# Performance work log

Measured on AMD Instinct MI355X. Metric: run time of the kernel, lower is better.

The kernel has to match this reference:

```python
import jax, jax.numpy as jnp
import numpy as np

B, N, C, H = 2, 8192, 256, 8  # Dh == C (attention_head_size = embedding_channels)
EPS = 1e-5  # InstanceNorm2d default eps


def setup_inputs() -> dict:
    key = jax.random.key(0)
    k1, k2, k3, k4, k5 = jax.random.split(key, 5)
    s = 1.0 / np.sqrt(C)
    return {
        "emb": jax.random.normal(k1, (B, N, C), dtype=jnp.float32),
        "Wq": jax.random.normal(k2, (C, C * H), dtype=jnp.float32) * s,
        "Wk": jax.random.normal(k3, (C, C * H), dtype=jnp.float32) * s,
        "Wv": jax.random.normal(k4, (C, C * H), dtype=jnp.float32) * s,
        "Wo": jax.random.normal(k5, (C * H, C), dtype=jnp.float32) * s,
    }


def reference(emb, Wq, Wk, Wv, Wo):
    b, n, c = emb.shape
    h = Wq.shape[1] // c  # num_heads; head_dim Dh == c

    def heads(x):  # [B,N,H*Dh] -> [B,H,N,Dh]
        return x.reshape(b, n, h, c).transpose(0, 2, 1, 3)

    qh = heads(emb @ Wq)  # [B,H,N,Dh]
    kh = heads(emb @ Wk)
    vh = heads(emb @ Wv)

    # channel attention: contract over sequence dim N -> [B,H,Dh,Dh]
    attn = jnp.einsum("bhnd,bhne->bhde", qh, kh)

    # InstanceNorm2d over the Dh x Dh map per (b,h), affine=False, biased var
    mu = attn.mean(axis=(2, 3), keepdims=True)
    var = attn.var(axis=(2, 3), keepdims=True)
    attn = (attn - mu) * jax.lax.rsqrt(var + EPS)

    attn = jax.nn.softmax(attn, axis=3)

    # attn @ v^T -> [B,H,Dh,N]
    ctx = jnp.einsum("bhde,bhne->bhdn", attn, vh)

    # permute(0,3,2,1) -> [B,N,Dh,H], flatten (Dh,H) -> KV_size
    ctx = ctx.transpose(0, 3, 2, 1).reshape(b, n, c * h)
    return ctx @ Wo  # [B,N,C]
```

## Files before the change

### kernel.cpp

```cpp
#include <hip/hip_runtime.h>
#include <hip/hip_bf16.h>

#define NB 2
#define NN 8192
#define NC 256
#define NH 8
#define NCH 2048

static constexpr float EPS = 1e-5f;


typedef __attribute__((ext_vector_type(8))) short bf16x8;
typedef __attribute__((ext_vector_type(4))) float f32x4;

#define MFMA16(a, b, c) __builtin_amdgcn_mfma_f32_16x16x32_bf16(a, b, c, 0, 0, 0)

static constexpr int ETH  = 0;
static constexpr int ETL  = 4194304;
static constexpr int WQTH = 8388608;
static constexpr int WQTL = 8912896;
static constexpr int WKTH = 9437184;
static constexpr int WKTL = 9961472;
static constexpr int WVH  = 10485760;
static constexpr int WVL  = 11010048;
static constexpr int WORH = 11534336;
static constexpr int WORL = 12058624;
static constexpr int GHH  = 12582912;
static constexpr int GHL  = 12713984;
static constexpr int T1H  = 12845056;
static constexpr int T1L  = 13893632;
static constexpr int SMH  = 14942208;
static constexpr int SML  = 15990784;
static constexpr int PTH  = 17039360;
static constexpr int PTL  = 17170432;


__device__ __forceinline__ ushort bf16rn(float x) {
    uint u = __float_as_uint(x);
    return (ushort)((u + 0x7fffu + ((u >> 16) & 1u)) >> 16);
}
__device__ __forceinline__ float bf2f(ushort h) { return __uint_as_float(((uint)h) << 16); }

__device__ __forceinline__ void stage64(ushort* __restrict__ lds, const ushort* __restrict__ src,
                                        int row0, int k0, int ld) {
    int t = threadIdx.x;
    int g = t & 7, r = t >> 3;
#pragma unroll
    for (int i = 0; i < 2; ++i, r += 32) {
        uint4 v = *(const uint4*)(src + (row0 + r) * ld + k0 + g * 8);
        *(uint4*)((char*)lds + r * 128 + ((g ^ (r & 7)) << 4)) = v;
    }
}

__device__ __forceinline__ void stage64_f32(ushort* __restrict__ ldsh, ushort* __restrict__ ldsl,
                                            const float* __restrict__ src, int row0, int k0, int ld) {
    int t = threadIdx.x;
    int g = t & 15, r = t >> 4;
#pragma unroll
    for (int i = 0; i < 4; ++i, r += 16) {
        float4 v = *(const float4*)(src + (row0 + r) * ld + k0 + g * 4);
        ushort h0 = bf16rn(v.x), h1 = bf16rn(v.y), h2 = bf16rn(v.z), h3 = bf16rn(v.w);
        ushort e0 = bf16rn(v.x - bf2f(h0)), e1 = bf16rn(v.y - bf2f(h1));
        ushort e2 = bf16rn(v.z - bf2f(h2)), e3 = bf16rn(v.w - bf2f(h3));
        int byte = r * 128 + ((((g >> 1) ^ (r & 7)) << 4) | ((g & 1) << 3));
        ushort4 hv = {h0, h1, h2, h3}, lv = {e0, e1, e2, e3};
        *(ushort4*)((char*)ldsh + byte) = hv;
        *(ushort4*)((char*)ldsl + byte) = lv;
    }
}

__device__ __forceinline__ bf16x8 frag64(const ushort* __restrict__ lds, int rbase, int ks) {
    int l = threadIdx.x & 63;
    int r = rbase + (l & 15);
    int slot = (ks * 4 + (l >> 4)) ^ (r & 7);
    return *(const bf16x8*)((const char*)lds + r * 128 + slot * 16);
}

__device__ __forceinline__ void mac3(f32x4& acc, bf16x8 ah, bf16x8 al, bf16x8 bh, bf16x8 bl) {
    acc = MFMA16(ah, bh, acc);
    acc = MFMA16(ah, bl, acc);
    acc = MFMA16(al, bh, acc);
}

__device__ __forceinline__ void mfma_tile(const ushort* Ah, const ushort* Al,
                                          const ushort* Bh, const ushort* Bl,
                                          int wm, int wn, f32x4 acc[2][2]) {
#pragma unroll
    for (int ks = 0; ks < 2; ++ks) {
        bf16x8 ah[2], al[2], bh[2], bl[2];
        ah[0] = frag64(Ah, wm, ks);      ah[1] = frag64(Ah, wm + 16, ks);
        al[0] = frag64(Al, wm, ks);      al[1] = frag64(Al, wm + 16, ks);
        bh[0] = frag64(Bh, wn, ks);      bh[1] = frag64(Bh, wn + 16, ks);
        bl[0] = frag64(Bl, wn, ks);      bl[1] = frag64(Bl, wn + 16, ks);
#pragma unroll
        for (int mi = 0; mi < 2; ++mi)
#pragma unroll
            for (int ni = 0; ni < 2; ++ni)
                mac3(acc[mi][ni], ah[mi], al[mi], bh[ni], bl[ni]);
    }
}

__device__ __forceinline__ void gemm_core(const ushort* Ahi, const ushort* Alo, int arow0, int lda, int k0a,
                                          const ushort* Bhi, const ushort* Blo, int brow0, int ldb, int k0b,
                                          int nkt, ushort* lds, f32x4 acc[2][2]) {
    ushort* Ah = lds; ushort* Al = lds + 4096; ushort* Bh = lds + 8192; ushort* Bl = lds + 12288;
    int w = threadIdx.x >> 6;
    int wm = (w >> 1) * 32, wn = (w & 1) * 32;
    for (int t = 0; t < nkt; ++t) {
        stage64(Ah, Ahi, arow0, k0a + t * 64, lda);
        stage64(Al, Alo, arow0, k0a + t * 64, lda);
        stage64(Bh, Bhi, brow0, k0b + t * 64, ldb);
        stage64(Bl, Blo, brow0, k0b + t * 64, ldb);
        __syncthreads();
        mfma_tile(Ah, Al, Bh, Bl, wm, wn, acc);
        __syncthreads();
    }
}

__device__ __forceinline__ void ep_hilo(ushort* Dh, ushort* Dl, int ld, int row0, int col0, f32x4 acc[2][2]) {
    int l = threadIdx.x & 63, w = threadIdx.x >> 6;
    int wm = (w >> 1) * 32, wn = (w & 1) * 32;
#pragma unroll
    for (int mi = 0; mi < 2; ++mi)
#pragma unroll
        for (int ni = 0; ni < 2; ++ni)
#pragma unroll
            for (int r = 0; r < 4; ++r) {
                float x = acc[mi][ni][r];
                int idx = (row0 + wm + mi * 16 + (l >> 4) * 4 + r) * ld + col0 + wn + ni * 16 + (l & 15);
                ushort h = bf16rn(x);
                Dh[idx] = h;
                Dl[idx] = bf16rn(x - bf2f(h));
            }
}

__device__ __forceinline__ void ep_f32(float* D, int ld, int row0, int col0, f32x4 acc[2][2]) {
    int l = threadIdx.x & 63, w = threadIdx.x >> 6;
    int wm = (w >> 1) * 32, wn = (w & 1) * 32;
#pragma unroll
    for (int mi = 0; mi < 2; ++mi)
#pragma unroll
        for (int ni = 0; ni < 2; ++ni)
#pragma unroll
            for (int r = 0; r < 4; ++r)
                D[(row0 + wm + mi * 16 + (l >> 4) * 4 + r) * ld + col0 + wn + ni * 16 + (l & 15)] = acc[mi][ni][r];
}

__device__ __forceinline__ void tsplit(uint (*lds)[65], const float* __restrict__ src, int srcStride,
                                       ushort* __restrict__ DH, ushort* __restrict__ DL) {
    int t = threadIdx.x;
    int r = t >> 4, g = t & 15;
#pragma unroll
    for (int i = 0; i < 4; ++i) {
        int m = r + i * 16;
        float4 v = *(const float4*)(src + m * srcStride + g * 4);
        ushort h;
        h = bf16rn(v.x); lds[g * 4 + 0][m] = h | ((uint)bf16rn(v.x - bf2f(h)) << 16);
        h = bf16rn(v.y); lds[g * 4 + 1][m] = h | ((uint)bf16rn(v.y - bf2f(h)) << 16);
        h = bf16rn(v.z); lds[g * 4 + 2][m] = h | ((uint)bf16rn(v.z - bf2f(h)) << 16);
        h = bf16rn(v.w); lds[g * 4 + 3][m] = h | ((uint)bf16rn(v.w - bf2f(h)) << 16);
    }
    __syncthreads();
    int j = t >> 3, q = t & 7;
#pragma unroll
    for (int i = 0; i < 2; ++i) {
        int jj = j + i * 32;
        uint a0 = lds[jj][q * 8 + 0], a1 = lds[jj][q * 8 + 1], a2 = lds[jj][q * 8 + 2], a3 = lds[jj][q * 8 + 3];
        uint a4 = lds[jj][q * 8 + 4], a5 = lds[jj][q * 8 + 5], a6 = lds[jj][q * 8 + 6], a7 = lds[jj][q * 8 + 7];
        uint4 hv = {(a0 & 0xffffu) | (a1 << 16), (a2 & 0xffffu) | (a3 << 16),
                    (a4 & 0xffffu) | (a5 << 16), (a6 & 0xffffu) | (a7 << 16)};
        uint4 lv = {(a0 >> 16) | (a1 & 0xffff0000u), (a2 >> 16) | (a3 & 0xffff0000u),
                    (a4 >> 16) | (a5 & 0xffff0000u), (a6 >> 16) | (a7 & 0xffff0000u)};
        *(uint4*)(DH + jj * NC + q * 8) = hv;
        *(uint4*)(DL + jj * NC + q * 8) = lv;
    }
}


__global__ __launch_bounds__(256) void k_prep(const float* __restrict__ wq, const float* __restrict__ wk,
                                              const float* __restrict__ wv, const float* __restrict__ wo,
                                              ushort* __restrict__ us, float* __restrict__ stats) {
    __shared__ uint lds[64][65];
    int x = blockIdx.x, z = blockIdx.y;
    int t = threadIdx.x;
    if (z == 3) {
        if (x == 0 && t < 64) stats[t] = 0.f;
        int i = (x * 256 + t) * 4;
        float4 v = *(const float4*)(wv + i);
        ushort h0 = bf16rn(v.x), h1 = bf16rn(v.y), h2 = bf16rn(v.z), h3 = bf16rn(v.w);
        ushort e0 = bf16rn(v.x - bf2f(h0)), e1 = bf16rn(v.y - bf2f(h1));
        ushort e2 = bf16rn(v.z - bf2f(h2)), e3 = bf16rn(v.w - bf2f(h3));
        ushort4 hv = {h0, h1, h2, h3}, lv = {e0, e1, e2, e3};
        *(ushort4*)(us + WVH + i) = hv;
        *(ushort4*)(us + WVL + i) = lv;
        return;
    }
    if (x >= 128) return;
    if (z == 2) {
        int h = x >> 4, dt = (x >> 2) & 3, jt = x & 3;
        tsplit(lds, wo + (dt * 64 * 8 + h) * NC + jt * 64, 8 * NC,
               us + WORH + h * 65536 + (jt * 64) * NC + dt * 64,
               us + WORL + h * 65536 + (jt * 64) * NC + dt * 64);
        return;
    }
    int jt = x >> 2, ct = x & 3;
    const float* W = z ? wk : wq;
    int dh = (z ? WKTH : WQTH) + (jt * 64) * NC + ct * 64;
    int dl = (z ? WKTL : WQTL) + (jt * 64) * NC + ct * 64;
    tsplit(lds, W + (ct * 64) * NCH + jt * 64, NCH, us + dh, us + dl);
}

__global__ __launch_bounds__(256) void k_s0(const float* __restrict__ emb, ushort* __restrict__ us) {
    __shared__ uint lds[64][65];
    int nt = blockIdx.x, ct = blockIdx.y, b = blockIdx.z;
    int t = threadIdx.x;
    const float* E = emb + b * (NN * NC);
    int n0 = nt * 64, c0 = ct * 64;
    int r = t >> 4, g = t & 15;
#pragma unroll
    for (int i = 0; i < 4; ++i) {
        int n = r + i * 16;
        float4 v = *(const float4*)(E + (n0 + n) * NC + c0 + g * 4);
        ushort h;
        h = bf16rn(v.x); lds[g * 4 + 0][n] = h | ((uint)bf16rn(v.x - bf2f(h)) << 16);
        h = bf16rn(v.y); lds[g * 4 + 1][n] = h | ((uint)bf16rn(v.y - bf2f(h)) << 16);
        h = bf16rn(v.z); lds[g * 4 + 2][n] = h | ((uint)bf16rn(v.z - bf2f(h)) << 16);
        h = bf16rn(v.w); lds[g * 4 + 3][n] = h | ((uint)bf16rn(v.w - bf2f(h)) << 16);
    }
    __syncthreads();
    ushort* EH = us + ETH + b * (NC * NN);
    ushort* EL = us + ETL + b * (NC * NN);
    int c = t >> 3, q = t & 7;
#pragma unroll
    for (int i = 0; i < 2; ++i) {
        int cc = c + i * 32;
        uint a0 = lds[cc][q * 8 + 0], a1 = lds[cc][q * 8 + 1], a2 = lds[cc][q * 8 + 2], a3 = lds[cc][q * 8 + 3];
        uint a4 = lds[cc][q * 8 + 4], a5 = lds[cc][q * 8 + 5], a6 = lds[cc][q * 8 + 6], a7 = lds[cc][q * 8 + 7];
        uint4 hv = {(a0 & 0xffffu) | (a1 << 16), (a2 & 0xffffu) | (a3 << 16),
                    (a4 & 0xffffu) | (a5 << 16), (a6 & 0xffffu) | (a7 << 16)};
        uint4 lv = {(a0 >> 16) | (a1 & 0xffff0000u), (a2 >> 16) | (a3 & 0xffff0000u),
                    (a4 >> 16) | (a5 & 0xffff0000u), (a6 >> 16) | (a7 & 0xffff0000u)};
        *(uint4*)(EH + (c0 + cc) * NN + n0 + q * 8) = hv;
        *(uint4*)(EL + (c0 + cc) * NN + n0 + q * 8) = lv;
    }
}

static __device__ const int TI1[10] = {0, 0, 0, 0, 1, 1, 1, 2, 2, 3};
static __device__ const int TI2[10] = {0, 1, 2, 3, 1, 2, 3, 2, 3, 3};

__global__ __launch_bounds__(256) void k_gram(const ushort* __restrict__ us, float* __restrict__ gp) {
    __shared__ ushort lds[16384];
    ushort* Ah = lds; ushort* Al = lds + 4096; ushort* Bh = lds + 8192; ushort* Bl = lds + 12288;
    int tile = blockIdx.x, kc = blockIdx.y, b = blockIdx.z;
    int c1 = TI1[tile] * 64, c2 = TI2[tile] * 64;
    bool diag = (c1 == c2);
    const ushort* eh = us + ETH + b * (NC * NN);
    const ushort* el = us + ETL + b * (NC * NN);
    int w = threadIdx.x >> 6;
    int wm = (w >> 1) * 32, wn = (w & 1) * 32;
    f32x4 acc[2][2] = {{{0.f, 0.f, 0.f, 0.f}, {0.f, 0.f, 0.f, 0.f}},
                       {{0.f, 0.f, 0.f, 0.f}, {0.f, 0.f, 0.f, 0.f}}};
    for (int kb = 0; kb < 8; ++kb) {
        int n0 = kc * 512 + kb * 64;
        stage64(Ah, eh, c1, n0, NN);
        stage64(Al, el, c1, n0, NN);
        if (!diag) { stage64(Bh, eh, c2, n0, NN); stage64(Bl, el, c2, n0, NN); }
        __syncthreads();
        mfma_tile(Ah, Al, diag ? Ah : Bh, diag ? Al : Bl, wm, wn, acc);
        __syncthreads();
    }
    ep_f32(gp + ((b * 16 + kc) * 10 + tile) * 4096, 64, 0, 0, acc);
}

__global__ __launch_bounds__(256) void k_s2(const float* __restrict__ gp, ushort* __restrict__ us) {
    __shared__ float T[64][65];
    int tile = blockIdx.x, b = blockIdx.y;
    int c1 = TI1[tile] * 64, c2 = TI2[tile] * 64;
    int t = threadIdx.x;
    const float* src = gp + (b * 160 + tile) * 4096;
    ushort* GH = us + GHH + b * 65536;
    ushort* GL = us + GHL + b * 65536;
    float4 s[4] = {{0.f, 0.f, 0.f, 0.f}, {0.f, 0.f, 0.f, 0.f}, {0.f, 0.f, 0.f, 0.f}, {0.f, 0.f, 0.f, 0.f}};
    for (int kc = 0; kc < 16; ++kc) {
        const float4* p = (const float4*)(src + kc * 40960);
#pragma unroll
        for (int k2 = 0; k2 < 4; ++k2) {
            float4 v = p[t + k2 * 256];
            s[k2].x += v.x; s[k2].y += v.y; s[k2].z += v.z; s[k2].w += v.w;
        }
    }
#pragma unroll
    for (int k2 = 0; k2 < 4; ++k2) {
        int f = t + k2 * 256;
        int r = f >> 4, c = (f & 15) * 4;
        ushort h0 = bf16rn(s[k2].x), h1 = bf16rn(s[k2].y), h2 = bf16rn(s[k2].z), h3 = bf16rn(s[k2].w);
        ushort e0 = bf16rn(s[k2].x - bf2f(h0)), e1 = bf16rn(s[k2].y - bf2f(h1));
        ushort e2 = bf16rn(s[k2].z - bf2f(h2)), e3 = bf16rn(s[k2].w - bf2f(h3));
        ushort4 hv = {h0, h1, h2, h3}, lv = {e0, e1, e2, e3};
        *(ushort4*)(GH + (c1 + r) * NC + c2 + c) = hv;
        *(ushort4*)(GL + (c1 + r) * NC + c2 + c) = lv;
        T[r][c + 0] = s[k2].x; T[r][c + 1] = s[k2].y; T[r][c + 2] = s[k2].z; T[r][c + 3] = s[k2].w;
    }
    if (c1 != c2) {
        __syncthreads();
#pragma unroll
        for (int k2 = 0; k2 < 4; ++k2) {
            int f = t + k2 * 256;
            int r = f >> 4, c = (f & 15) * 4;
            float a0 = T[c + 0][r], a1 = T[c + 1][r], a2 = T[c + 2][r], a3 = T[c + 3][r];
            ushort h0 = bf16rn(a0), h1 = bf16rn(a1), h2 = bf16rn(a2), h3 = bf16rn(a3);
            ushort e0 = bf16rn(a0 - bf2f(h0)), e1 = bf16rn(a1 - bf2f(h1));
            ushort e2 = bf16rn(a2 - bf2f(h2)), e3 = bf16rn(a3 - bf2f(h3));
            ushort4 hv = {h0, h1, h2, h3}, lv = {e0, e1, e2, e3};
            *(ushort4*)(GH + (c2 + r) * NC + c1 + c) = hv;
            *(ushort4*)(GL + (c2 + r) * NC + c1 + c) = lv;
        }
    }
}

__global__ __launch_bounds__(256) void k_t1(ushort* __restrict__ us) {
    __shared__ ushort lds[16384];
    int mt = blockIdx.x, nt = blockIdx.y, b = blockIdx.z;
    f32x4 acc[2][2] = {{{0.f, 0.f, 0.f, 0.f}, {0.f, 0.f, 0.f, 0.f}},
                       {{0.f, 0.f, 0.f, 0.f}, {0.f, 0.f, 0.f, 0.f}}};
    gemm_core(us + WQTH, us + WQTL, mt * 64, NC, 0,
              us + GHH + b * 65536, us + GHL + b * 65536, nt * 64, NC, 0, 4, lds, acc);
    ep_hilo(us + T1H + b * 524288, us + T1L + b * 524288, NC, mt * 64, nt * 64, acc);
}

__global__ __launch_bounds__(256) void k_attn(ushort* __restrict__ us, float* __restrict__ attn,
                                              float* __restrict__ stats) {
    __shared__ ushort lds[16384];
    int tile = blockIdx.x, bh = blockIdx.y;
    int b = bh >> 3, h = bh & 7;
    int row0 = (tile >> 2) * 64, col0 = (tile & 3) * 64;
    f32x4 acc[2][2] = {{{0.f, 0.f, 0.f, 0.f}, {0.f, 0.f, 0.f, 0.f}},
                       {{0.f, 0.f, 0.f, 0.f}, {0.f, 0.f, 0.f, 0.f}}};
    gemm_core(us + T1H + b * 524288, us + T1L + b * 524288, h * 256 + row0, NC, 0,
              us + WKTH, us + WKTL, h * 256 + col0, NC, 0, 4, lds, acc);
    float* D = attn + bh * 65536;
    int l = threadIdx.x & 63, w = threadIdx.x >> 6;
    int wm = (w >> 1) * 32, wn = (w & 1) * 32;
    float lsum = 0.f, lss = 0.f;
#pragma unroll
    for (int mi = 0; mi < 2; ++mi)
#pragma unroll
        for (int ni = 0; ni < 2; ++ni)
#pragma unroll
            for (int r = 0; r < 4; ++r) {
                float x = acc[mi][ni][r];
                D[(row0 + wm + mi * 16 + (l >> 4) * 4 + r) * NC + col0 + wn + ni * 16 + (l & 15)] = x;
                lsum += x; lss += x * x;
            }
#pragma unroll
    for (int o = 32; o > 0; o >>= 1) { lsum += __shfl_xor(lsum, o); lss += __shfl_xor(lss, o); }
    if (l == 0) { atomicAdd(&stats[bh * 2], lsum); atomicAdd(&stats[bh * 2 + 1], lss); }
}

__global__ __launch_bounds__(256) void k_sm(const float* __restrict__ attn, const float* __restrict__ stats,
                                            ushort* __restrict__ us) {
    int bh = blockIdx.x, rb = blockIdx.y;
    float mean = stats[bh * 2] * (1.f / 65536.f);
    float var = stats[bh * 2 + 1] * (1.f / 65536.f) - mean * mean;
    float rs = rsqrtf(var + EPS);
    int w = threadIdx.x >> 6, l = threadIdx.x & 63;
    const float* src = attn + bh * 65536;
    ushort* dh = us + SMH + bh * 65536;
    ushort* dl = us + SML + bh * 65536;
    for (int rr = 0; rr < 16; ++rr) {
        int row = rb * 64 + w * 16 + rr;
        float4 v = *(const float4*)(src + row * 256 + l * 4);
        v.x *= rs; v.y *= rs; v.z *= rs; v.w *= rs;
        float mx = fmaxf(fmaxf(v.x, v.y), fmaxf(v.z, v.w));
#pragma unroll
        for (int o = 32; o > 0; o >>= 1) mx = fmaxf(mx, __shfl_xor(mx, o));
        float e0 = __expf(v.x - mx), e1 = __expf(v.y - mx), e2 = __expf(v.z - mx), e3 = __expf(v.w - mx);
        float se = e0 + e1 + e2 + e3;
#pragma unroll
        for (int o = 32; o > 0; o >>= 1) se += __shfl_xor(se, o);
        float inv = 1.f / se;
        e0 *= inv; e1 *= inv; e2 *= inv; e3 *= inv;
        ushort h0 = bf16rn(e0), h1 = bf16rn(e1), h2 = bf16rn(e2), h3 = bf16rn(e3);
        ushort f0 = bf16rn(e0 - bf2f(h0)), f1 = bf16rn(e1 - bf2f(h1));
        ushort f2 = bf16rn(e2 - bf2f(h2)), f3 = bf16rn(e3 - bf2f(h3));
        ushort4 hv = {h0, h1, h2, h3}, lv = {f0, f1, f2, f3};
        *(ushort4*)(dh + row * 256 + l * 4) = hv;
        *(ushort4*)(dl + row * 256 + l * 4) = lv;
    }
}

__global__ __launch_bounds__(256) void k_m(ushort* __restrict__ us) {
    __shared__ ushort lds[16384];
    int tile = blockIdx.x, bh = blockIdx.y;
    int h = bh & 7;
    int c0 = (tile >> 2) * 64, d0 = (tile & 3) * 64;
    f32x4 acc[2][2] = {{{0.f, 0.f, 0.f, 0.f}, {0.f, 0.f, 0.f, 0.f}},
                       {{0.f, 0.f, 0.f, 0.f}, {0.f, 0.f, 0.f, 0.f}}};
    gemm_core(us + WVH, us + WVL, c0, NCH, h * 256,
              us + SMH + bh * 65536, us + SML + bh * 65536, d0, NC, 0, 4, lds, acc);
    ep_hilo(us + T1H + bh * 65536, us + T1L + bh * 65536, NC, c0, d0, acc);
}

__global__ __launch_bounds__(256) void k_pt(ushort* __restrict__ us, float* __restrict__ ptp) {
    __shared__ ushort lds[16384];
    int tile = blockIdx.x, bh = blockIdx.y;
    int h = bh & 7;
    int j0 = (tile >> 2) * 64, c0 = (tile & 3) * 64;
    f32x4 acc[2][2] = {{{0.f, 0.f, 0.f, 0.f}, {0.f, 0.f, 0.f, 0.f}},
                       {{0.f, 0.f, 0.f, 0.f}, {0.f, 0.f, 0.f, 0.f}}};
    gemm_core(us + WORH + h * 65536, us + WORL + h * 65536, j0, NC, 0,
              us + T1H + bh * 65536, us + T1L + bh * 65536, c0, NC, 0, 4, lds, acc);
    ep_f32(ptp + bh * 65536, NC, j0, c0, acc);
}

__global__ __launch_bounds__(256) void k_s4(const float* __restrict__ ptp, ushort* __restrict__ us) {
    int b = blockIdx.y;
    int i = (blockIdx.x * 256 + threadIdx.x) * 4;
    const float* src = ptp + b * 8 * 65536 + i;
    float4 s = {0.f, 0.f, 0.f, 0.f};
#pragma unroll
    for (int h = 0; h < 8; ++h) {
        float4 v = *(const float4*)(src + h * 65536);
        s.x += v.x; s.y += v.y; s.z += v.z; s.w += v.w;
    }
    ushort h0 = bf16rn(s.x), h1 = bf16rn(s.y), h2 = bf16rn(s.z), h3 = bf16rn(s.w);
    ushort e0 = bf16rn(s.x - bf2f(h0)), e1 = bf16rn(s.y - bf2f(h1));
    ushort e2 = bf16rn(s.z - bf2f(h2)), e3 = bf16rn(s.w - bf2f(h3));
    ushort4 hv = {h0, h1, h2, h3}, lv = {e0, e1, e2, e3};
    *(ushort4*)(us + PTH + b * 65536 + i) = hv;
    *(ushort4*)(us + PTL + b * 65536 + i) = lv;
}

__global__ __launch_bounds__(256) void k_out(const float* __restrict__ emb, const ushort* __restrict__ us,
                                             float* __restrict__ out) {
    __shared__ ushort lds[16384];
    ushort* Ah = lds; ushort* Al = lds + 4096; ushort* Bh = lds + 8192; ushort* Bl = lds + 12288;
    int nt = blockIdx.x, jt = blockIdx.y, b = blockIdx.z;
    const float* E = emb + b * (NN * NC);
    const ushort* PH = us + PTH + b * 65536;
    const ushort* PL = us + PTL + b * 65536;
    int w = threadIdx.x >> 6;
    int wm = (w >> 1) * 32, wn = (w & 1) * 32;
    f32x4 acc[2][2] = {{{0.f, 0.f, 0.f, 0.f}, {0.f, 0.f, 0.f, 0.f}},
                       {{0.f, 0.f, 0.f, 0.f}, {0.f, 0.f, 0.f, 0.f}}};
    for (int t = 0; t < 4; ++t) {
        stage64_f32(Ah, Al, E, nt * 64, t * 64, NC);
        stage64(Bh, PH, jt * 64, t * 64, NC);
        stage64(Bl, PL, jt * 64, t * 64, NC);
        __syncthreads();
        mfma_tile(Ah, Al, Bh, Bl, wm, wn, acc);
        __syncthreads();
    }
    ep_f32(out + b * (NN * NC), NC, nt * 64, jt * 64, acc);
}


extern "C" void kernel_launch(void* const* d_in, const int* in_sizes, int n_in,
                              void* d_out, int out_size, void* d_ws, size_t ws_size,
                              hipStream_t stream) {
    const float* emb = (const float*)d_in[0];
    const float* Wq  = (const float*)d_in[1];
    const float* Wk  = (const float*)d_in[2];
    const float* Wv  = (const float*)d_in[3];
    const float* Wo  = (const float*)d_in[4];
    float* out = (float*)d_out;
    float* ws  = (float*)d_ws;

    float* Gp    = ws;
    float* attn  = ws;
    float* Ptp   = ws + 1310720;
    float* stats = ws + 2359296;
    ushort* us   = (ushort*)(ws + 2359360);

    k_prep<<<dim3(512, 4),     dim3(256), 0, stream>>>(Wq, Wk, Wv, Wo, us, stats);
    k_s0  <<<dim3(128, 4, NB), dim3(256), 0, stream>>>(emb, us);
    k_gram<<<dim3(10, 16, NB), dim3(256), 0, stream>>>(us, Gp);
    k_s2  <<<dim3(10, NB),     dim3(256), 0, stream>>>(Gp, us);
    k_t1  <<<dim3(32, 4, NB),  dim3(256), 0, stream>>>(us);
    k_attn<<<dim3(16, 16),     dim3(256), 0, stream>>>(us, attn, stats);
    k_sm  <<<dim3(16, 4),      dim3(256), 0, stream>>>(attn, stats, us);
    k_m   <<<dim3(16, 16),     dim3(256), 0, stream>>>(us);
    k_pt  <<<dim3(16, 16),     dim3(256), 0, stream>>>(us, Ptp);
    k_s4  <<<dim3(64, NB),     dim3(256), 0, stream>>>(Ptp, us);
    k_out <<<dim3(128, 4, NB), dim3(256), 0, stream>>>(emb, us, out);
}
```

Before: 172.6 us.

## Merge emb split into prep, atomically reduce P, and widen gram/softmax grids

Folds the emb transpose/hi-lo split kernel into k_prep as extra grid planes, and has k_prep zero a P buffer. k_pt now accumulates per-head contributions into P with float atomics, which removes the k_s4 reduction kernel; k_out then splits P from fp32 itself. The Gram kernel gets twice as many K-chunks with half the depth each to raise parallelism, and the softmax kernel handles 4 rows per wave over a larger grid. Together these cut launches and intermediate traffic, at the cost of atomic contention, nondeterministic summation order, and a larger partial-sum reduction in k_s2.

```diff
diff --git a/kernel.cpp b/kernel.cpp
--- a/kernel.cpp
+++ b/kernel.cpp
@@ -31,8 +31,6 @@
 static constexpr int T1L  = 13893632;
 static constexpr int SMH  = 14942208;
 static constexpr int SML  = 15990784;
-static constexpr int PTH  = 17039360;
-static constexpr int PTL  = 17170432;
 
 
 __device__ __forceinline__ ushort bf16rn(float x) {
@@ -179,12 +177,47 @@
 
 __global__ __launch_bounds__(256) void k_prep(const float* __restrict__ wq, const float* __restrict__ wk,
                                               const float* __restrict__ wv, const float* __restrict__ wo,
-                                              ushort* __restrict__ us, float* __restrict__ stats) {
+                                              const float* __restrict__ emb, ushort* __restrict__ us,
+                                              float* __restrict__ P, float* __restrict__ stats) {
     __shared__ uint lds[64][65];
     int x = blockIdx.x, z = blockIdx.y;
     int t = threadIdx.x;
+    if (z >= 4) {
+        int b = z - 4, nt = x >> 2, ct = x & 3;
+        const float* E = emb + b * (NN * NC);
+        int n0 = nt * 64, c0 = ct * 64;
+        int r = t >> 4, g = t & 15;
+#pragma unroll
+        for (int i = 0; i < 4; ++i) {
+            int n = r + i * 16;
+            float4 v = *(const float4*)(E + (n0 + n) * NC + c0 + g * 4);
+            ushort h;
+            h = bf16rn(v.x); lds[g * 4 + 0][n] = h | ((uint)bf16rn(v.x - bf2f(h)) << 16);
+            h = bf16rn(v.y); lds[g * 4 + 1][n] = h | ((uint)bf16rn(v.y - bf2f(h)) << 16);
+            h = bf16rn(v.z); lds[g * 4 + 2][n] = h | ((uint)bf16rn(v.z - bf2f(h)) << 16);
+            h = bf16rn(v.w); lds[g * 4 + 3][n] = h | ((uint)bf16rn(v.w - bf2f(h)) << 16);
+        }
+        __syncthreads();
+        ushort* EH = us + ETH + b * (NC * NN);
+        ushort* EL = us + ETL + b * (NC * NN);
+        int c = t >> 3, q = t & 7;
+#pragma unroll
+        for (int i = 0; i < 2; ++i) {
+            int cc = c + i * 32;
+            uint a0 = lds[cc][q * 8 + 0], a1 = lds[cc][q * 8 + 1], a2 = lds[cc][q * 8 + 2], a3 = lds[cc][q * 8 + 3];
+            uint a4 = lds[cc][q * 8 + 4], a5 = lds[cc][q * 8 + 5], a6 = lds[cc][q * 8 + 6], a7 = lds[cc][q * 8 + 7];
+            uint4 hv = {(a0 & 0xffffu) | (a1 << 16), (a2 & 0xffffu) | (a3 << 16),
+                        (a4 & 0xffffu) | (a5 << 16), (a6 & 0xffffu) | (a7 << 16)};
+            uint4 lv = {(a0 >> 16) | (a1 & 0xffff0000u), (a2 >> 16) | (a3 & 0xffff0000u),
+                        (a4 >> 16) | (a5 & 0xffff0000u), (a6 >> 16) | (a7 & 0xffff0000u)};
+            *(uint4*)(EH + (c0 + cc) * NN + n0 + q * 8) = hv;
+            *(uint4*)(EL + (c0 + cc) * NN + n0 + q * 8) = lv;
+        }
+        return;
+    }
     if (z == 3) {
         if (x == 0 && t < 64) stats[t] = 0.f;
+        P[x * 256 + t] = 0.f;
         int i = (x * 256 + t) * 4;
         float4 v = *(const float4*)(wv + i);
         ushort h0 = bf16rn(v.x), h1 = bf16rn(v.y), h2 = bf16rn(v.z), h3 = bf16rn(v.w);
@@ -210,41 +243,6 @@
     tsplit(lds, W + (ct * 64) * NCH + jt * 64, NCH, us + dh, us + dl);
 }
 
-__global__ __launch_bounds__(256) void k_s0(const float* __restrict__ emb, ushort* __restrict__ us) {
-    __shared__ uint lds[64][65];
-    int nt = blockIdx.x, ct = blockIdx.y, b = blockIdx.z;
-    int t = threadIdx.x;
-    const float* E = emb + b * (NN * NC);
-    int n0 = nt * 64, c0 = ct * 64;
-    int r = t >> 4, g = t & 15;
-#pragma unroll
-    for (int i = 0; i < 4; ++i) {
-        int n = r + i * 16;
-        float4 v = *(const float4*)(E + (n0 + n) * NC + c0 + g * 4);
-        ushort h;
-        h = bf16rn(v.x); lds[g * 4 + 0][n] = h | ((uint)bf16rn(v.x - bf2f(h)) << 16);
-        h = bf16rn(v.y); lds[g * 4 + 1][n] = h | ((uint)bf16rn(v.y - bf2f(h)) << 16);
-        h = bf16rn(v.z); lds[g * 4 + 2][n] = h | ((uint)bf16rn(v.z - bf2f(h)) << 16);
-        h = bf16rn(v.w); lds[g * 4 + 3][n] = h | ((uint)bf16rn(v.w - bf2f(h)) << 16);
-    }
-    __syncthreads();
-    ushort* EH = us + ETH + b * (NC * NN);
-    ushort* EL = us + ETL + b * (NC * NN);
-    int c = t >> 3, q = t & 7;
-#pragma unroll
-    for (int i = 0; i < 2; ++i) {
-        int cc = c + i * 32;
-        uint a0 = lds[cc][q * 8 + 0], a1 = lds[cc][q * 8 + 1], a2 = lds[cc][q * 8 + 2], a3 = lds[cc][q * 8 + 3];
-        uint a4 = lds[cc][q * 8 + 4], a5 = lds[cc][q * 8 + 5], a6 = lds[cc][q * 8 + 6], a7 = lds[cc][q * 8 + 7];
-        uint4 hv = {(a0 & 0xffffu) | (a1 << 16), (a2 & 0xffffu) | (a3 << 16),
-                    (a4 & 0xffffu) | (a5 << 16), (a6 & 0xffffu) | (a7 << 16)};
-        uint4 lv = {(a0 >> 16) | (a1 & 0xffff0000u), (a2 >> 16) | (a3 & 0xffff0000u),
-                    (a4 >> 16) | (a5 & 0xffff0000u), (a6 >> 16) | (a7 & 0xffff0000u)};
-        *(uint4*)(EH + (c0 + cc) * NN + n0 + q * 8) = hv;
-        *(uint4*)(EL + (c0 + cc) * NN + n0 + q * 8) = lv;
-    }
-}
-
 static __device__ const int TI1[10] = {0, 0, 0, 0, 1, 1, 1, 2, 2, 3};
 static __device__ const int TI2[10] = {0, 1, 2, 3, 1, 2, 3, 2, 3, 3};
 
@@ -260,8 +258,8 @@
     int wm = (w >> 1) * 32, wn = (w & 1) * 32;
     f32x4 acc[2][2] = {{{0.f, 0.f, 0.f, 0.f}, {0.f, 0.f, 0.f, 0.f}},
                        {{0.f, 0.f, 0.f, 0.f}, {0.f, 0.f, 0.f, 0.f}}};
-    for (int kb = 0; kb < 8; ++kb) {
-        int n0 = kc * 512 + kb * 64;
+    for (int kb = 0; kb < 4; ++kb) {
+        int n0 = kc * 256 + kb * 64;
         stage64(Ah, eh, c1, n0, NN);
         stage64(Al, el, c1, n0, NN);
         if (!diag) { stage64(Bh, eh, c2, n0, NN); stage64(Bl, el, c2, n0, NN); }
@@ -269,7 +267,7 @@
         mfma_tile(Ah, Al, diag ? Ah : Bh, diag ? Al : Bl, wm, wn, acc);
         __syncthreads();
     }
-    ep_f32(gp + ((b * 16 + kc) * 10 + tile) * 4096, 64, 0, 0, acc);
+    ep_f32(gp + ((b * 32 + kc) * 10 + tile) * 4096, 64, 0, 0, acc);
 }
 
 __global__ __launch_bounds__(256) void k_s2(const float* __restrict__ gp, ushort* __restrict__ us) {
@@ -277,11 +275,11 @@
     int tile = blockIdx.x, b = blockIdx.y;
     int c1 = TI1[tile] * 64, c2 = TI2[tile] * 64;
     int t = threadIdx.x;
-    const float* src = gp + (b * 160 + tile) * 4096;
+    const float* src = gp + (b * 320 + tile) * 4096;
     ushort* GH = us + GHH + b * 65536;
     ushort* GL = us + GHL + b * 65536;
     float4 s[4] = {{0.f, 0.f, 0.f, 0.f}, {0.f, 0.f, 0.f, 0.f}, {0.f, 0.f, 0.f, 0.f}, {0.f, 0.f, 0.f, 0.f}};
-    for (int kc = 0; kc < 16; ++kc) {
+    for (int kc = 0; kc < 32; ++kc) {
         const float4* p = (const float4*)(src + kc * 40960);
 #pragma unroll
         for (int k2 = 0; k2 < 4; ++k2) {
@@ -312,8 +310,8 @@
             ushort e0 = bf16rn(a0 - bf2f(h0)), e1 = bf16rn(a1 - bf2f(h1));
             ushort e2 = bf16rn(a2 - bf2f(h2)), e3 = bf16rn(a3 - bf2f(h3));
             ushort4 hv = {h0, h1, h2, h3}, lv = {e0, e1, e2, e3};
-            *(ushort4*)(GH + (c2 + r) * NC + c1 + c) = hv;
-            *(ushort4*)(GL + (c2 + r) * NC + c1 + c) = lv;
+            *(uint4*)(GH + (c2 + r) * NC + c1 + c) = *(uint4*)&hv;
+            *(uint4*)(GL + (c2 + r) * NC + c1 + c) = *(uint4*)&lv;
         }
     }
 }
@@ -367,8 +365,9 @@
     const float* src = attn + bh * 65536;
     ushort* dh = us + SMH + bh * 65536;
     ushort* dl = us + SML + bh * 65536;
-    for (int rr = 0; rr < 16; ++rr) {
-        int row = rb * 64 + w * 16 + rr;
+#pragma unroll
+    for (int rr = 0; rr < 4; ++rr) {
+        int row = rb * 16 + w * 4 + rr;
         float4 v = *(const float4*)(src + row * 256 + l * 4);
         v.x *= rs; v.y *= rs; v.z *= rs; v.w *= rs;
         float mx = fmaxf(fmaxf(v.x, v.y), fmaxf(v.z, v.w));
@@ -401,52 +400,42 @@
     ep_hilo(us + T1H + bh * 65536, us + T1L + bh * 65536, NC, c0, d0, acc);
 }
 
-__global__ __launch_bounds__(256) void k_pt(ushort* __restrict__ us, float* __restrict__ ptp) {
+__global__ __launch_bounds__(256) void k_pt(ushort* __restrict__ us, float* __restrict__ P) {
     __shared__ ushort lds[16384];
     int tile = blockIdx.x, bh = blockIdx.y;
-    int h = bh & 7;
+    int b = bh >> 3, h = bh & 7;
     int j0 = (tile >> 2) * 64, c0 = (tile & 3) * 64;
     f32x4 acc[2][2] = {{{0.f, 0.f, 0.f, 0.f}, {0.f, 0.f, 0.f, 0.f}},
                        {{0.f, 0.f, 0.f, 0.f}, {0.f, 0.f, 0.f, 0.f}}};
     gemm_core(us + WORH + h * 65536, us + WORL + h * 65536, j0, NC, 0,
               us + T1H + bh * 65536, us + T1L + bh * 65536, c0, NC, 0, 4, lds, acc);
-    ep_f32(ptp + bh * 65536, NC, j0, c0, acc);
-}
-
-__global__ __launch_bounds__(256) void k_s4(const float* __restrict__ ptp, ushort* __restrict__ us) {
-    int b = blockIdx.y;
-    int i = (blockIdx.x * 256 + threadIdx.x) * 4;
-    const float* src = ptp + b * 8 * 65536 + i;
-    float4 s = {0.f, 0.f, 0.f, 0.f};
-#pragma unroll
-    for (int h = 0; h < 8; ++h) {
-        float4 v = *(const float4*)(src + h * 65536);
-        s.x += v.x; s.y += v.y; s.z += v.z; s.w += v.w;
-    }
-    ushort h0 = bf16rn(s.x), h1 = bf16rn(s.y), h2 = bf16rn(s.z), h3 = bf16rn(s.w);
-    ushort e0 = bf16rn(s.x - bf2f(h0)), e1 = bf16rn(s.y - bf2f(h1));
-    ushort e2 = bf16rn(s.z - bf2f(h2)), e3 = bf16rn(s.w - bf2f(h3));
-    ushort4 hv = {h0, h1, h2, h3}, lv = {e0, e1, e2, e3};
-    *(ushort4*)(us + PTH + b * 65536 + i) = hv;
-    *(ushort4*)(us + PTL + b * 65536 + i) = lv;
-}
-
-__global__ __launch_bounds__(256) void k_out(const float* __restrict__ emb, const ushort* __restrict__ us,
+    float* D = P + b * 65536;
+    int l = threadIdx.x & 63, w = threadIdx.x >> 6;
+    int wm = (w >> 1) * 32, wn = (w & 1) * 32;
+#pragma unroll
+    for (int mi = 0; mi < 2; ++mi)
+#pragma unroll
+        for (int ni = 0; ni < 2; ++ni)
+#pragma unroll
+            for (int r = 0; r < 4; ++r)
+                atomicAdd(&D[(j0 + wm + mi * 16 + (l >> 4) * 4 + r) * NC + c0 + wn + ni * 16 + (l & 15)],
+                          acc[mi][ni][r]);
+}
+
+__global__ __launch_bounds__(256) void k_out(const float* __restrict__ emb, const float* __restrict__ P,
                                              float* __restrict__ out) {
     __shared__ ushort lds[16384];
     ushort* Ah = lds; ushort* Al = lds + 4096; ushort* Bh = lds + 8192; ushort* Bl = lds + 12288;
     int nt = blockIdx.x, jt = blockIdx.y, b = blockIdx.z;
     const float* E = emb + b * (NN * NC);
-    const ushort* PH = us + PTH + b * 65536;
-    const ushort* PL = us + PTL + b * 65536;
+    const float* Pb = P + b * 65536;
     int w = threadIdx.x >> 6;
     int wm = (w >> 1) * 32, wn = (w & 1) * 32;
     f32x4 acc[2][2] = {{{0.f, 0.f, 0.f, 0.f}, {0.f, 0.f, 0.f, 0.f}},
                        {{0.f, 0.f, 0.f, 0.f}, {0.f, 0.f, 0.f, 0.f}}};
     for (int t = 0; t < 4; ++t) {
         stage64_f32(Ah, Al, E, nt * 64, t * 64, NC);
-        stage64(Bh, PH, jt * 64, t * 64, NC);
-        stage64(Bl, PL, jt * 64, t * 64, NC);
+        stage64_f32(Bh, Bl, Pb, jt * 64, t * 64, NC);
         __syncthreads();
         mfma_tile(Ah, Al, Bh, Bl, wm, wn, acc);
         __syncthreads();
@@ -468,19 +457,17 @@
 
     float* Gp    = ws;
     float* attn  = ws;
-    float* Ptp   = ws + 1310720;
-    float* stats = ws + 2359296;
-    ushort* us   = (ushort*)(ws + 2359360);
-
-    k_prep<<<dim3(512, 4),     dim3(256), 0, stream>>>(Wq, Wk, Wv, Wo, us, stats);
-    k_s0  <<<dim3(128, 4, NB), dim3(256), 0, stream>>>(emb, us);
-    k_gram<<<dim3(10, 16, NB), dim3(256), 0, stream>>>(us, Gp);
+    float* P     = ws + 2621440;
+    float* stats = ws + 2752512;
+    ushort* us   = (ushort*)(ws + 2752576);
+
+    k_prep<<<dim3(512, 6),     dim3(256), 0, stream>>>(Wq, Wk, Wv, Wo, emb, us, P, stats);
+    k_gram<<<dim3(10, 32, NB), dim3(256), 0, stream>>>(us, Gp);
     k_s2  <<<dim3(10, NB),     dim3(256), 0, stream>>>(Gp, us);
     k_t1  <<<dim3(32, 4, NB),  dim3(256), 0, stream>>>(us);
     k_attn<<<dim3(16, 16),     dim3(256), 0, stream>>>(us, attn, stats);
-    k_sm  <<<dim3(16, 4),      dim3(256), 0, stream>>>(attn, stats, us);
+    k_sm  <<<dim3(16, 16),     dim3(256), 0, stream>>>(attn, stats, us);
     k_m   <<<dim3(16, 16),     dim3(256), 0, stream>>>(us);
-    k_pt  <<<dim3(16, 16),     dim3(256), 0, stream>>>(us, Ptp);
-    k_s4  <<<dim3(64, NB),     dim3(256), 0, stream>>>(Ptp, us);
-    k_out <<<dim3(128, 4, NB), dim3(256), 0, stream>>>(emb, us, out);
-}
+    k_pt  <<<dim3(16, 16),     dim3(256), 0, stream>>>(us, P);
+    k_out <<<dim3(128, 4, NB), dim3(256), 0, stream>>>(emb, P, out);
+}
```

After: 165.7 us. -4.0%, faster.
